# Optimization experiments

Measured on AMD Instinct MI355X. Metric: run time of the kernel, lower is better.

## Reference

```python
import jax, jax.numpy as jnp
import numpy as np
from jax import lax

LBDA = 0.1
EPS = 0.01
NUM_CLASSES = 20


def setup_inputs() -> dict:
    key = jax.random.key(0)
    k1, k2 = jax.random.split(key)
    target_features = jax.random.normal(k1, (2048, 8, 2048), dtype=jnp.float32)
    support_features = jax.random.normal(k2, (100, 8, 2048), dtype=jnp.float32)
    # 20-way 5-shot: every class present so per-class mean is well defined
    support_labels = jnp.repeat(jnp.arange(NUM_CLASSES, dtype=jnp.int32), 100 // NUM_CLASSES)
    return {
        "target_features": target_features,
        "support_features": support_features,
        "support_labels": support_labels,
    }


def _softmin(xs, lbda):
    # -lbda * log(sum_i exp(-x_i/lbda)), stable
    return -lbda * jax.nn.logsumexp(jnp.stack([-x / lbda for x in xs], axis=0), axis=0)


def otam_cum_dist(dists, lbda=LBDA):
    # dists: [Q, Sp, L, S] frame distance matrices
    d = jnp.pad(dists, ((0, 0), (0, 0), (0, 0), (1, 1)))  # pad columns -> M = S + 2
    M = d.shape[-1]
    # row 0: running sum along columns (cum[0,0] = d[0,0] = 0 from padding)
    row0 = jnp.cumsum(d[:, :, 0, :], axis=-1)

    def step(prev_row, d_row):
        # prev_row, d_row: [Q, Sp, M]; column 0 is never written -> stays 0
        cur = [jnp.zeros_like(d_row[..., 0])]
        cur.append(d_row[..., 1] + _softmin([prev_row[..., 0], prev_row[..., 1], cur[0]], lbda))
        for m in range(2, M - 1):
            cur.append(d_row[..., m] + _softmin([prev_row[..., m - 1], cur[m - 1]], lbda))
        cur.append(d_row[..., M - 1] + _softmin([prev_row[..., M - 2], prev_row[..., M - 1], cur[M - 2]], lbda))
        new_row = jnp.stack(cur, axis=-1)
        return new_row, None

    d_rows = jnp.moveaxis(d[:, :, 1:, :], 2, 0)  # [L-1, Q, Sp, M]
    final_row, _ = lax.scan(step, row0, d_rows)
    return final_row[..., -1]  # [Q, Sp]


def cos_sim(x, y, eps=EPS):
    num = x @ y.T
    den = jnp.linalg.norm(x, axis=-1)[:, None] * jnp.linalg.norm(y, axis=-1)[None, :] + eps
    return num / den


def reference(target_features, support_features, support_labels):
    Q, S, D = target_features.shape
    Sp = support_features.shape[0]
    tf = target_features.reshape(Q * S, D)
    sf = support_features.reshape(Sp * S, D)
    frame_dists = 1.0 - cos_sim(tf, sf)  # [Q*S, Sp*S]
    # '(tb ts) (sb ss) -> tb sb ts ss'
    dists = frame_dists.reshape(Q, S, Sp, S).transpose(0, 2, 1, 3)
    cum_dists = otam_cum_dist(dists) + otam_cum_dist(dists.transpose(0, 1, 3, 2))  # [Q, Sp]
    # per-class mean over support (torch.unique returns sorted labels 0..C-1)
    onehot = (support_labels[:, None] == jnp.arange(NUM_CLASSES)[None, :]).astype(cum_dists.dtype)
    onehot = onehot / jnp.sum(onehot, axis=0, keepdims=True)
    class_dists = cum_dists @ onehot  # [Q, C]
    return -class_dists[None]  # logits [1, Q, C]
```

## Files before the change

kernel.cpp:

```cpp
#include <hip/hip_runtime.h>

#define QN    2048
#define SS    8
#define DD    2048
#define SP    100
#define NCLS  20
#define MROWS (QN*SS)
#define NROWS (SP*SS)
#define NPAD  800
#define KK    DD

typedef __bf16 bf16x8 __attribute__((ext_vector_type(8)));
typedef float  f32x4  __attribute__((ext_vector_type(4)));

__device__ __forceinline__ unsigned short f2bf(float f) {
    unsigned int u = __float_as_uint(f);
    u += 0x7fffu + ((u >> 16) & 1u);
    return (unsigned short)(u >> 16);
}

__global__ void cvt_kernel(const float* __restrict__ tf, const float* __restrict__ sf,
                           unsigned short* __restrict__ Abf, unsigned short* __restrict__ Bbf,
                           float* __restrict__ nA, float* __restrict__ nB,
                           float* __restrict__ out)
{
    if (blockIdx.x < 160) out[blockIdx.x * 256 + threadIdx.x] = 0.f;

    const int wv   = threadIdx.x >> 6;
    const int lane = threadIdx.x & 63;
    const int row  = blockIdx.x * 4 + wv;

    const float* src;
    unsigned short* dst;
    float* nrm; int r;
    if (row < MROWS) { src = tf + (size_t)row * DD; dst = Abf + (size_t)row * DD; nrm = nA; r = row; }
    else {
        r = row - MROWS;
        src = sf + (size_t)r * DD; dst = Bbf + (size_t)r * DD; nrm = nB;
    }

    float s = 0.f;
#pragma unroll
    for (int j = 0; j < 8; j++) {
        float4 v = *(const float4*)(src + j * 256 + lane * 4);
        s += v.x*v.x + v.y*v.y + v.z*v.z + v.w*v.w;
        ushort4 pk = make_ushort4(f2bf(v.x), f2bf(v.y), f2bf(v.z), f2bf(v.w));
        *(ushort4*)(dst + j * 256 + lane * 4) = pk;
    }
#pragma unroll
    for (int o = 32; o; o >>= 1) s += __shfl_down(s, o);
    if (lane == 0) nrm[r] = sqrtf(s);
}

__device__ __forceinline__ float softmin2(float a, float b) {
    float mn = fminf(a, b), mx = fmaxf(a, b);
    return mn - 0.1f * __logf(1.0f + __expf((mn - mx) * 10.0f));
}
__device__ __forceinline__ float softmin3(float a, float b, float c) {
    float mn = fminf(fminf(a, b), c);
    float sum = __expf((mn - a) * 10.0f) + __expf((mn - b) * 10.0f) + __expf((mn - c) * 10.0f);
    return mn - 0.1f * __logf(sum);
}

__device__ __forceinline__ void gld16(const void* g, void* l) {
    __builtin_amdgcn_global_load_lds(
        (const __attribute__((address_space(1))) unsigned int*)g,
        (__attribute__((address_space(3))) unsigned int*)l, 16, 0, 0);
}

__device__ __forceinline__ float cellf(const uint4* raw, int a, int b) {
    const unsigned* p = (const unsigned*)raw;
    unsigned wv = p[a * 4 + (b >> 1)];
    return __uint_as_float((b & 1) ? (wv & 0xffff0000u) : (wv << 16));
}

__device__ __forceinline__ float otam_dp(const uint4* raw, int dir) {
    float prev[10], cur[10];
    prev[0] = 0.f;
#pragma unroll
    for (int m = 1; m <= 8; m++) {
        float v0 = cellf(raw, 0, m - 1), v1 = cellf(raw, m - 1, 0);
        prev[m] = prev[m - 1] + (dir ? v1 : v0);
    }
    prev[9] = prev[8];
#pragma unroll
    for (int l = 1; l < 8; l++) {
        float d[8];
#pragma unroll
        for (int j = 0; j < 8; j++) {
            float v0 = cellf(raw, l, j), v1 = cellf(raw, j, l);
            d[j] = dir ? v1 : v0;
        }
        cur[1] = d[0] + softmin3(prev[0], prev[1], 0.0f);
#pragma unroll
        for (int m = 2; m <= 8; m++)
            cur[m] = d[m - 1] + softmin2(prev[m - 1], cur[m - 1]);
        cur[9] = softmin3(prev[8], prev[9], cur[8]);
#pragma unroll
        for (int m = 1; m < 10; m++) prev[m] = cur[m];
    }
    return prev[9];
}

#define EBS (32 * 72)

__global__ __launch_bounds__(256, 2) void gemm_kernel(
    const unsigned short* __restrict__ A,
    const unsigned short* __restrict__ B,
    const float* __restrict__ nA, const float* __restrict__ nB,
    const int* __restrict__ labels,
    float* __restrict__ out)
{
    __shared__ __align__(16) unsigned short smem[4 * EBS];
    unsigned short* Als = smem;
    unsigned short* Bls = smem + 4096;

    const int mt  = blockIdx.x;
    const int nt  = blockIdx.y;
    const int tid = threadIdx.x;
    const int lane = tid & 63;
    const int w    = tid >> 6;
    const int col  = lane & 15, kg = lane >> 4;
    const int mbase0 = mt * 128;

    const int c0 = tid, c1 = tid + 256;
    const unsigned short* Ab0 = A + (size_t)(mbase0 + (c0 >> 2)) * KK + (c0 & 3) * 8;
    const unsigned short* Ab1 = A + (size_t)(mbase0 + (c1 >> 2)) * KK + (c1 & 3) * 8;

    if (nt < 6) {
        const int wm = (w & 1) * 64, wn = (w >> 1) * 64;
        f32x4 acc[4][4] = {};
        const unsigned short* Bb0 = B + (size_t)(nt * 128 + (c0 >> 2)) * KK + (c0 & 3) * 8;
        const unsigned short* Bb1 = B + (size_t)(nt * 128 + (c1 >> 2)) * KK + (c1 & 3) * 8;

        for (int kk = 0; kk < KK; kk += 32) {
            __syncthreads();
            gld16(Ab0 + kk, (char*)Als + c0 * 16);
            gld16(Ab1 + kk, (char*)Als + c1 * 16);
            gld16(Bb0 + kk, (char*)Bls + c0 * 16);
            gld16(Bb1 + kk, (char*)Bls + c1 * 16);
            __syncthreads();
            bf16x8 af[4], bfr[4];
#pragma unroll
            for (int i = 0; i < 4; i++) af[i]  = *(const bf16x8*)(Als + (wm + i * 16 + col) * 32 + kg * 8);
#pragma unroll
            for (int i = 0; i < 4; i++) bfr[i] = *(const bf16x8*)(Bls + (wn + i * 16 + col) * 32 + kg * 8);
#pragma unroll
            for (int mi = 0; mi < 4; mi++)
#pragma unroll
                for (int ni = 0; ni < 4; ni++)
                    acc[mi][ni] = __builtin_amdgcn_mfma_f32_16x16x32_bf16(af[mi], bfr[ni], acc[mi][ni], 0, 0, 0);
        }

        __syncthreads();
        unsigned short* eb = smem + w * EBS;
        const int mbase = mbase0 + wm;
        const int nbase = nt * 128 + wn;
        const int pr  = lane & 31;
        const int qv2 = pr >> 3, sv = pr & 7;
        const int dir = lane >> 5;

#pragma unroll
        for (int p = 0; p < 2; p++) {
            if (p) __syncthreads();
#pragma unroll
            for (int mi2 = 0; mi2 < 2; mi2++) {
                const int mi = p * 2 + mi2;
                float nx[4];
#pragma unroll
                for (int r = 0; r < 4; r++) nx[r] = nA[mbase + mi * 16 + kg * 4 + r];
#pragma unroll
                for (int ni = 0; ni < 4; ni++) {
                    const float ny = nB[nbase + ni * 16 + col];
#pragma unroll
                    for (int r = 0; r < 4; r++) {
                        float d = 1.0f - acc[mi][ni][r] * __builtin_amdgcn_rcpf(nx[r] * ny + 0.01f);
                        eb[(mi2 * 16 + kg * 4 + r) * 72 + ni * 16 + col] = f2bf(d);
                    }
                }
            }
            __syncthreads();

            uint4 raw[8];
            const unsigned short* tb = eb + (qv2 * 8) * 72 + sv * 8;
#pragma unroll
            for (int l = 0; l < 8; l++) raw[l] = *(const uint4*)(tb + l * 72);

            float res = otam_dp(raw, dir);
            res += __shfl_down(res, 32);
            if (dir == 0) {
                const int qg = mt * 16 + (wm >> 3) + p * 4 + qv2;
                const int sg = nt * 16 + (wn >> 3) + sv;
                atomicAdd(out + (size_t)qg * NCLS + labels[sg], -res * 0.2f);
            }
        }
    } else {
        const int wm = w * 32;
        f32x4 acc[2][2] = {};
        const unsigned short* Bb0 = B + (size_t)(768 + (tid >> 2)) * KK + (tid & 3) * 8;

        for (int kk = 0; kk < KK; kk += 32) {
            __syncthreads();
            gld16(Ab0 + kk, (char*)Als + c0 * 16);
            gld16(Ab1 + kk, (char*)Als + c1 * 16);
            if (tid < 128) gld16(Bb0 + kk, (char*)Bls + tid * 16);
            __syncthreads();
            bf16x8 af[2], bfr[2];
#pragma unroll
            for (int i = 0; i < 2; i++) af[i]  = *(const bf16x8*)(Als + (wm + i * 16 + col) * 32 + kg * 8);
#pragma unroll
            for (int i = 0; i < 2; i++) bfr[i] = *(const bf16x8*)(Bls + (i * 16 + col) * 32 + kg * 8);
#pragma unroll
            for (int mi = 0; mi < 2; mi++)
#pragma unroll
                for (int ni = 0; ni < 2; ni++)
                    acc[mi][ni] = __builtin_amdgcn_mfma_f32_16x16x32_bf16(af[mi], bfr[ni], acc[mi][ni], 0, 0, 0);
        }

        __syncthreads();
        unsigned short* eb = smem + w * EBS;
        const int mbase = mbase0 + wm;

#pragma unroll
        for (int mi = 0; mi < 2; mi++) {
            float nx[4];
#pragma unroll
            for (int r = 0; r < 4; r++) nx[r] = nA[mbase + mi * 16 + kg * 4 + r];
#pragma unroll
            for (int ni = 0; ni < 2; ni++) {
                const float ny = nB[768 + ni * 16 + col];
#pragma unroll
                for (int r = 0; r < 4; r++) {
                    float d = 1.0f - acc[mi][ni][r] * __builtin_amdgcn_rcpf(nx[r] * ny + 0.01f);
                    eb[(mi * 16 + kg * 4 + r) * 40 + ni * 16 + col] = f2bf(d);
                }
            }
        }
        __syncthreads();

        const int pr  = lane & 31;
        const int qv2 = (pr & 15) >> 2, sv = pr & 3;
        const int dir = lane >> 5;
        uint4 raw[8];
        const unsigned short* tb = eb + (qv2 * 8) * 40 + sv * 8;
#pragma unroll
        for (int l = 0; l < 8; l++) raw[l] = *(const uint4*)(tb + l * 40);

        float res = otam_dp(raw, dir);
        res += __shfl_down(res, 32);
        if (dir == 0 && pr < 16) {
            const int qg = mt * 16 + w * 4 + qv2;
            const int sg = 96 + sv;
            atomicAdd(out + (size_t)qg * NCLS + labels[sg], -res * 0.2f);
        }
    }
}

extern "C" void kernel_launch(void* const* d_in, const int* in_sizes, int n_in,
                              void* d_out, int out_size, void* d_ws, size_t ws_size,
                              hipStream_t stream)
{
    const float* tf     = (const float*)d_in[0];
    const float* sf     = (const float*)d_in[1];
    const int*   labels = (const int*)d_in[2];
    float* out = (float*)d_out;

    char* ws = (char*)d_ws;
    const size_t szA    = (size_t)MROWS * KK * 2;
    const size_t szB    = (size_t)NPAD  * KK * 2;
    const size_t szNA   = (size_t)MROWS * 4;
    unsigned short* Abf = (unsigned short*)ws;
    unsigned short* Bbf = (unsigned short*)(ws + szA);
    float* nA   = (float*)(ws + szA + szB);
    float* nB   = (float*)(ws + szA + szB + szNA);

    cvt_kernel<<<(MROWS + NPAD) / 4, 256, 0, stream>>>(tf, sf, Abf, Bbf, nA, nB, out);
    gemm_kernel<<<dim3(MROWS / 128, 7), 256, 0, stream>>>(Abf, Bbf, nA, nB, labels, out);
}
```

Baseline: 279.4 us.

## Use 256x256 double-buffered swizzled LDS GEMM tile with padded support rows

Replaces the 128x128 BK=32 GEMM and its separate remainder path with a single 512-thread kernel using 256x256 tiles, BK=64 and double-buffered, XOR-swizzled LDS. Global-to-LDS loads for the next k-step are interleaved with MFMA phases, using fine-grained waitcnt, barriers and setprio. The support matrix is zero-padded to 1024 rows so every tile is full, and out-of-range support columns are masked at the atomic stage. This trades extra padded MMA work and 128KB of dynamic LDS per block for higher data reuse and latency hiding.

New measurement: 281.9 us. Within noise of the previous version (+0.9%).

```diff
diff --git a/kernel.cpp b/kernel.cpp
--- a/kernel.cpp
+++ b/kernel.cpp
@@ -6,9 +6,11 @@
 #define SP    100
 #define NCLS  20
 #define MROWS (QN*SS)
-#define NROWS (SP*SS)
-#define NPAD  800
+#define NREAL (SP*SS)
+#define NPAD  1024
 #define KK    DD
+#define BK    64
+#define NTK   (KK/BK)
 
 typedef __bf16 bf16x8 __attribute__((ext_vector_type(8)));
 typedef float  f32x4  __attribute__((ext_vector_type(4)));
@@ -36,6 +38,14 @@
     if (row < MROWS) { src = tf + (size_t)row * DD; dst = Abf + (size_t)row * DD; nrm = nA; r = row; }
     else {
         r = row - MROWS;
+        if (r >= NREAL) {
+            unsigned short* d2 = Bbf + (size_t)r * DD;
+            ushort4 z = make_ushort4(0, 0, 0, 0);
+#pragma unroll
+            for (int j = 0; j < 8; ++j) *(ushort4*)(d2 + j * 256 + lane * 4) = z;
+            if (lane == 0) nB[r] = 0.f;
+            return;
+        }
         src = sf + (size_t)r * DD; dst = Bbf + (size_t)r * DD; nrm = nB;
     }
 
@@ -102,156 +112,180 @@
     return prev[9];
 }
 
-#define EBS (32 * 72)
-
-__global__ __launch_bounds__(256, 2) void gemm_kernel(
+__global__ __launch_bounds__(512, 2) void gemm_kernel(
     const unsigned short* __restrict__ A,
     const unsigned short* __restrict__ B,
     const float* __restrict__ nA, const float* __restrict__ nB,
     const int* __restrict__ labels,
     float* __restrict__ out)
 {
-    __shared__ __align__(16) unsigned short smem[4 * EBS];
-    unsigned short* Als = smem;
-    unsigned short* Bls = smem + 4096;
-
-    const int mt  = blockIdx.x;
-    const int nt  = blockIdx.y;
-    const int tid = threadIdx.x;
+    extern __shared__ __align__(16) char lds8[];
+
+    const int mt   = blockIdx.x;
+    const int nt   = blockIdx.y;
+    const int tid  = threadIdx.x;
     const int lane = tid & 63;
     const int w    = tid >> 6;
+    const int wm   = w >> 2, wn = w & 3;
     const int col  = lane & 15, kg = lane >> 4;
-    const int mbase0 = mt * 128;
-
-    const int c0 = tid, c1 = tid + 256;
-    const unsigned short* Ab0 = A + (size_t)(mbase0 + (c0 >> 2)) * KK + (c0 & 3) * 8;
-    const unsigned short* Ab1 = A + (size_t)(mbase0 + (c1 >> 2)) * KK + (c1 & 3) * 8;
-
-    if (nt < 6) {
-        const int wm = (w & 1) * 64, wn = (w >> 1) * 64;
-        f32x4 acc[4][4] = {};
-        const unsigned short* Bb0 = B + (size_t)(nt * 128 + (c0 >> 2)) * KK + (c0 & 3) * 8;
-        const unsigned short* Bb1 = B + (size_t)(nt * 128 + (c1 >> 2)) * KK + (c1 & 3) * 8;
-
-        for (int kk = 0; kk < KK; kk += 32) {
-            __syncthreads();
-            gld16(Ab0 + kk, (char*)Als + c0 * 16);
-            gld16(Ab1 + kk, (char*)Als + c1 * 16);
-            gld16(Bb0 + kk, (char*)Bls + c0 * 16);
-            gld16(Bb1 + kk, (char*)Bls + c1 * 16);
-            __syncthreads();
-            bf16x8 af[4], bfr[4];
-#pragma unroll
-            for (int i = 0; i < 4; i++) af[i]  = *(const bf16x8*)(Als + (wm + i * 16 + col) * 32 + kg * 8);
-#pragma unroll
-            for (int i = 0; i < 4; i++) bfr[i] = *(const bf16x8*)(Bls + (wn + i * 16 + col) * 32 + kg * 8);
-#pragma unroll
-            for (int mi = 0; mi < 4; mi++)
-#pragma unroll
-                for (int ni = 0; ni < 4; ni++)
-                    acc[mi][ni] = __builtin_amdgcn_mfma_f32_16x16x32_bf16(af[mi], bfr[ni], acc[mi][ni], 0, 0, 0);
-        }
-
-        __syncthreads();
-        unsigned short* eb = smem + w * EBS;
-        const int mbase = mbase0 + wm;
-        const int nbase = nt * 128 + wn;
-        const int pr  = lane & 31;
-        const int qv2 = pr >> 3, sv = pr & 7;
-        const int dir = lane >> 5;
-
-#pragma unroll
-        for (int p = 0; p < 2; p++) {
-            if (p) __syncthreads();
-#pragma unroll
-            for (int mi2 = 0; mi2 < 2; mi2++) {
-                const int mi = p * 2 + mi2;
-                float nx[4];
-#pragma unroll
-                for (int r = 0; r < 4; r++) nx[r] = nA[mbase + mi * 16 + kg * 4 + r];
-#pragma unroll
-                for (int ni = 0; ni < 4; ni++) {
-                    const float ny = nB[nbase + ni * 16 + col];
-#pragma unroll
-                    for (int r = 0; r < 4; r++) {
-                        float d = 1.0f - acc[mi][ni][r] * __builtin_amdgcn_rcpf(nx[r] * ny + 0.01f);
-                        eb[(mi2 * 16 + kg * 4 + r) * 72 + ni * 16 + col] = f2bf(d);
-                    }
+    const int mbase = mt * 256, nbase = nt * 256;
+
+    const int ks8 = ((lane & 7) ^ (lane >> 3)) << 3;
+    const unsigned short* sA = A + (size_t)(mbase + w * 8 + (lane >> 3)) * KK + ks8;
+    const unsigned short* sB = B + (size_t)(nbase + w * 8 + (lane >> 3)) * KK + ks8;
+    const int stoff = w * 1024 + lane * 16;
+
+    const int sb16 = ((kg ^ (col & 7)) << 4);
+    const int arow = (wm * 128 + col) * 128;
+    const int brow = 32768 + (wn * 64 + col) * 128;
+
+    f32x4 acc[8][4] = {};
+
+    gld16(sB,                       lds8 + 32768 + stoff);
+    gld16(sB + (size_t) 64 * KK,    lds8 + 32768 +  8192 + stoff);
+    gld16(sB + (size_t)128 * KK,    lds8 + 32768 + 16384 + stoff);
+    gld16(sB + (size_t)192 * KK,    lds8 + 32768 + 24576 + stoff);
+    gld16(sA,                       lds8 + stoff);
+    gld16(sA + (size_t)128 * KK,    lds8 + 16384 + stoff);
+    gld16(sA + (size_t) 64 * KK,    lds8 +  8192 + stoff);
+    gld16(sA + (size_t)192 * KK,    lds8 + 24576 + stoff);
+    asm volatile("s_waitcnt vmcnt(0)" ::: "memory");
+    __builtin_amdgcn_s_barrier();
+
+    for (int t = 0; t < NTK; ++t) {
+        const int cb = (t & 1) << 16;
+        const int nb = cb ^ 65536;
+        const bool st = (t + 1 < NTK);
+        const int t1 = (t + 1) * BK;
+        bf16x8 af[4], bf0[4], bf1[4];
+
+#pragma unroll
+        for (int i = 0; i < 4; ++i)
+            af[i]  = *(const bf16x8*)(lds8 + cb + arow + i * 2048 + sb16);
+#pragma unroll
+        for (int n = 0; n < 4; ++n)
+            bf0[n] = *(const bf16x8*)(lds8 + cb + brow + n * 2048 + sb16);
+        if (st) {
+            gld16(sB + t1,                    lds8 + nb + 32768 + stoff);
+            gld16(sB + (size_t) 64 * KK + t1, lds8 + nb + 32768 +  8192 + stoff);
+            gld16(sB + (size_t)128 * KK + t1, lds8 + nb + 32768 + 16384 + stoff);
+            gld16(sB + (size_t)192 * KK + t1, lds8 + nb + 32768 + 24576 + stoff);
+        }
+        __builtin_amdgcn_s_barrier();
+        asm volatile("s_waitcnt lgkmcnt(0)" ::: "memory");
+        __builtin_amdgcn_sched_barrier(0);
+        __builtin_amdgcn_s_setprio(1);
+#pragma unroll
+        for (int mi = 0; mi < 4; ++mi)
+#pragma unroll
+            for (int n = 0; n < 4; ++n)
+                acc[mi][n] = __builtin_amdgcn_mfma_f32_16x16x32_bf16(af[mi], bf0[n], acc[mi][n], 0, 0, 0);
+        __builtin_amdgcn_s_setprio(0);
+        __builtin_amdgcn_sched_barrier(0);
+        __builtin_amdgcn_s_barrier();
+
+#pragma unroll
+        for (int i = 0; i < 4; ++i)
+            af[i]  = *(const bf16x8*)(lds8 + cb + arow + i * 2048 + (sb16 ^ 64));
+#pragma unroll
+        for (int n = 0; n < 4; ++n)
+            bf1[n] = *(const bf16x8*)(lds8 + cb + brow + n * 2048 + (sb16 ^ 64));
+        if (st) {
+            gld16(sA + t1,                    lds8 + nb + stoff);
+            gld16(sA + (size_t)128 * KK + t1, lds8 + nb + 16384 + stoff);
+        }
+        asm volatile("s_waitcnt vmcnt(6)" ::: "memory");
+        __builtin_amdgcn_s_barrier();
+        asm volatile("s_waitcnt lgkmcnt(0)" ::: "memory");
+        __builtin_amdgcn_sched_barrier(0);
+        __builtin_amdgcn_s_setprio(1);
+#pragma unroll
+        for (int mi = 0; mi < 4; ++mi)
+#pragma unroll
+            for (int n = 0; n < 4; ++n)
+                acc[mi][n] = __builtin_amdgcn_mfma_f32_16x16x32_bf16(af[mi], bf1[n], acc[mi][n], 0, 0, 0);
+        __builtin_amdgcn_s_setprio(0);
+        __builtin_amdgcn_sched_barrier(0);
+        __builtin_amdgcn_s_barrier();
+
+#pragma unroll
+        for (int i = 0; i < 4; ++i)
+            af[i] = *(const bf16x8*)(lds8 + cb + arow + 8192 + i * 2048 + sb16);
+        if (st) {
+            gld16(sA + (size_t) 64 * KK + t1, lds8 + nb +  8192 + stoff);
+            gld16(sA + (size_t)192 * KK + t1, lds8 + nb + 24576 + stoff);
+        }
+        __builtin_amdgcn_s_barrier();
+        asm volatile("s_waitcnt lgkmcnt(0)" ::: "memory");
+        __builtin_amdgcn_sched_barrier(0);
+        __builtin_amdgcn_s_setprio(1);
+#pragma unroll
+        for (int mi = 0; mi < 4; ++mi)
+#pragma unroll
+            for (int n = 0; n < 4; ++n)
+                acc[4 + mi][n] = __builtin_amdgcn_mfma_f32_16x16x32_bf16(af[mi], bf0[n], acc[4 + mi][n], 0, 0, 0);
+        __builtin_amdgcn_s_setprio(0);
+        __builtin_amdgcn_sched_barrier(0);
+        __builtin_amdgcn_s_barrier();
+
+#pragma unroll
+        for (int i = 0; i < 4; ++i)
+            af[i] = *(const bf16x8*)(lds8 + cb + arow + 8192 + i * 2048 + (sb16 ^ 64));
+        asm volatile("s_waitcnt vmcnt(2)" ::: "memory");
+        __builtin_amdgcn_s_barrier();
+        asm volatile("s_waitcnt lgkmcnt(0)" ::: "memory");
+        __builtin_amdgcn_sched_barrier(0);
+        __builtin_amdgcn_s_setprio(1);
+#pragma unroll
+        for (int mi = 0; mi < 4; ++mi)
+#pragma unroll
+            for (int n = 0; n < 4; ++n)
+                acc[4 + mi][n] = __builtin_amdgcn_mfma_f32_16x16x32_bf16(af[mi], bf1[n], acc[4 + mi][n], 0, 0, 0);
+        __builtin_amdgcn_s_setprio(0);
+        __builtin_amdgcn_sched_barrier(0);
+        __builtin_amdgcn_s_barrier();
+    }
+
+    __syncthreads();
+    unsigned short* eb = (unsigned short*)lds8 + w * 2304;
+    const int pr  = lane & 31;
+    const int qv2 = pr >> 3, sv = pr & 7;
+    const int dir = lane >> 5;
+
+#pragma unroll
+    for (int p = 0; p < 4; ++p) {
+        if (p) __syncthreads();
+#pragma unroll
+        for (int mi2 = 0; mi2 < 2; ++mi2) {
+            const int mi = p * 2 + mi2;
+            float nx[4];
+#pragma unroll
+            for (int r = 0; r < 4; ++r) nx[r] = nA[mbase + wm * 128 + mi * 16 + kg * 4 + r];
+#pragma unroll
+            for (int ni = 0; ni < 4; ++ni) {
+                const float ny = nB[nbase + wn * 64 + ni * 16 + col];
+#pragma unroll
+                for (int r = 0; r < 4; ++r) {
+                    float d = 1.0f - acc[mi][ni][r] * __builtin_amdgcn_rcpf(nx[r] * ny + 0.01f);
+                    eb[(mi2 * 16 + kg * 4 + r) * 72 + ni * 16 + col] = f2bf(d);
                 }
             }
-            __syncthreads();
-
-            uint4 raw[8];
-            const unsigned short* tb = eb + (qv2 * 8) * 72 + sv * 8;
-#pragma unroll
-            for (int l = 0; l < 8; l++) raw[l] = *(const uint4*)(tb + l * 72);
-
-            float res = otam_dp(raw, dir);
-            res += __shfl_down(res, 32);
-            if (dir == 0) {
-                const int qg = mt * 16 + (wm >> 3) + p * 4 + qv2;
-                const int sg = nt * 16 + (wn >> 3) + sv;
+        }
+        __syncthreads();
+
+        uint4 raw[8];
+        const unsigned short* tb = eb + (qv2 * 8) * 72 + sv * 8;
+#pragma unroll
+        for (int l = 0; l < 8; ++l) raw[l] = *(const uint4*)(tb + l * 72);
+
+        float res = otam_dp(raw, dir);
+        res += __shfl_down(res, 32);
+        if (dir == 0) {
+            const int sg = nt * 32 + wn * 8 + sv;
+            if (sg < SP) {
+                const int qg = mt * 32 + wm * 16 + p * 4 + qv2;
                 atomicAdd(out + (size_t)qg * NCLS + labels[sg], -res * 0.2f);
             }
-        }
-    } else {
-        const int wm = w * 32;
-        f32x4 acc[2][2] = {};
-        const unsigned short* Bb0 = B + (size_t)(768 + (tid >> 2)) * KK + (tid & 3) * 8;
-
-        for (int kk = 0; kk < KK; kk += 32) {
-            __syncthreads();
-            gld16(Ab0 + kk, (char*)Als + c0 * 16);
-            gld16(Ab1 + kk, (char*)Als + c1 * 16);
-            if (tid < 128) gld16(Bb0 + kk, (char*)Bls + tid * 16);
-            __syncthreads();
-            bf16x8 af[2], bfr[2];
-#pragma unroll
-            for (int i = 0; i < 2; i++) af[i]  = *(const bf16x8*)(Als + (wm + i * 16 + col) * 32 + kg * 8);
-#pragma unroll
-            for (int i = 0; i < 2; i++) bfr[i] = *(const bf16x8*)(Bls + (i * 16 + col) * 32 + kg * 8);
-#pragma unroll
-            for (int mi = 0; mi < 2; mi++)
-#pragma unroll
-                for (int ni = 0; ni < 2; ni++)
-                    acc[mi][ni] = __builtin_amdgcn_mfma_f32_16x16x32_bf16(af[mi], bfr[ni], acc[mi][ni], 0, 0, 0);
-        }
-
-        __syncthreads();
-        unsigned short* eb = smem + w * EBS;
-        const int mbase = mbase0 + wm;
-
-#pragma unroll
-        for (int mi = 0; mi < 2; mi++) {
-            float nx[4];
-#pragma unroll
-            for (int r = 0; r < 4; r++) nx[r] = nA[mbase + mi * 16 + kg * 4 + r];
-#pragma unroll
-            for (int ni = 0; ni < 2; ni++) {
-                const float ny = nB[768 + ni * 16 + col];
-#pragma unroll
-                for (int r = 0; r < 4; r++) {
-                    float d = 1.0f - acc[mi][ni][r] * __builtin_amdgcn_rcpf(nx[r] * ny + 0.01f);
-                    eb[(mi * 16 + kg * 4 + r) * 40 + ni * 16 + col] = f2bf(d);
-                }
-            }
-        }
-        __syncthreads();
-
-        const int pr  = lane & 31;
-        const int qv2 = (pr & 15) >> 2, sv = pr & 3;
-        const int dir = lane >> 5;
-        uint4 raw[8];
-        const unsigned short* tb = eb + (qv2 * 8) * 40 + sv * 8;
-#pragma unroll
-        for (int l = 0; l < 8; l++) raw[l] = *(const uint4*)(tb + l * 40);
-
-        float res = otam_dp(raw, dir);
-        res += __shfl_down(res, 32);
-        if (dir == 0 && pr < 16) {
-            const int qg = mt * 16 + w * 4 + qv2;
-            const int sg = 96 + sv;
-            atomicAdd(out + (size_t)qg * NCLS + labels[sg], -res * 0.2f);
         }
     }
 }
@@ -274,6 +308,13 @@
     float* nA   = (float*)(ws + szA + szB);
     float* nB   = (float*)(ws + szA + szB + szNA);
 
+    static int inited = 0;
+    if (!inited) {
+        (void)hipFuncSetAttribute((const void*)gemm_kernel,
+                                  hipFuncAttributeMaxDynamicSharedMemorySize, 131072);
+        inited = 1;
+    }
+
     cvt_kernel<<<(MROWS + NPAD) / 4, 256, 0, stream>>>(tf, sf, Abf, Bbf, nA, nB, out);
-    gemm_kernel<<<dim3(MROWS / 128, 7), 256, 0, stream>>>(Abf, Bbf, nA, nB, labels, out);
-}
+    gemm_kernel<<<dim3(MROWS / 256, NPAD / 256), 512, 131072, stream>>>(Abf, Bbf, nA, nB, labels, out);
+}
```

## Swizzle LDS k-chunks with XOR and remap block order for L2 locality

Applied to the files above, without the earlier changes.

Global-to-LDS loads now place each 16-byte k-chunk at a position XORed with the row index, and the fragment reads use the matching XOR. This is meant to remove LDS bank conflicts when a wavefront reads 16 rows at the same k offset. Block indices are also remapped so that consecutive blocks, spread across the 8 interleaved groups, cover neighbouring M tiles and all N tiles. The aim is better L2/MALL reuse of the A and B tiles. The remap assumes a grid of 128 by 7 blocks.

After: 289.5 us. 3.6% more time.

```diff
diff --git a/kernel.cpp b/kernel.cpp
--- a/kernel.cpp
+++ b/kernel.cpp
@@ -115,23 +115,26 @@
     unsigned short* Als = smem;
     unsigned short* Bls = smem + 4096;
 
-    const int mt  = blockIdx.x;
-    const int nt  = blockIdx.y;
+    const int d   = blockIdx.y * 128 + blockIdx.x;
+    const int s   = (d & 7) * 112 + (d >> 3);
+    const int mt  = s / 7;
+    const int nt  = s % 7;
     const int tid = threadIdx.x;
     const int lane = tid & 63;
     const int w    = tid >> 6;
     const int col  = lane & 15, kg = lane >> 4;
+    const int kgs  = kg ^ (col & 3);
     const int mbase0 = mt * 128;
 
     const int c0 = tid, c1 = tid + 256;
-    const unsigned short* Ab0 = A + (size_t)(mbase0 + (c0 >> 2)) * KK + (c0 & 3) * 8;
-    const unsigned short* Ab1 = A + (size_t)(mbase0 + (c1 >> 2)) * KK + (c1 & 3) * 8;
+    const unsigned short* Ab0 = A + (size_t)(mbase0 + (c0 >> 2)) * KK + (((c0 & 3) ^ ((c0 >> 2) & 3)) * 8);
+    const unsigned short* Ab1 = A + (size_t)(mbase0 + (c1 >> 2)) * KK + (((c1 & 3) ^ ((c1 >> 2) & 3)) * 8);
 
     if (nt < 6) {
         const int wm = (w & 1) * 64, wn = (w >> 1) * 64;
         f32x4 acc[4][4] = {};
-        const unsigned short* Bb0 = B + (size_t)(nt * 128 + (c0 >> 2)) * KK + (c0 & 3) * 8;
-        const unsigned short* Bb1 = B + (size_t)(nt * 128 + (c1 >> 2)) * KK + (c1 & 3) * 8;
+        const unsigned short* Bb0 = B + (size_t)(nt * 128 + (c0 >> 2)) * KK + (((c0 & 3) ^ ((c0 >> 2) & 3)) * 8);
+        const unsigned short* Bb1 = B + (size_t)(nt * 128 + (c1 >> 2)) * KK + (((c1 & 3) ^ ((c1 >> 2) & 3)) * 8);
 
         for (int kk = 0; kk < KK; kk += 32) {
             __syncthreads();
@@ -142,9 +145,9 @@
             __syncthreads();
             bf16x8 af[4], bfr[4];
 #pragma unroll
-            for (int i = 0; i < 4; i++) af[i]  = *(const bf16x8*)(Als + (wm + i * 16 + col) * 32 + kg * 8);
-#pragma unroll
-            for (int i = 0; i < 4; i++) bfr[i] = *(const bf16x8*)(Bls + (wn + i * 16 + col) * 32 + kg * 8);
+            for (int i = 0; i < 4; i++) af[i]  = *(const bf16x8*)(Als + (wm + i * 16 + col) * 32 + kgs * 8);
+#pragma unroll
+            for (int i = 0; i < 4; i++) bfr[i] = *(const bf16x8*)(Bls + (wn + i * 16 + col) * 32 + kgs * 8);
 #pragma unroll
             for (int mi = 0; mi < 4; mi++)
 #pragma unroll
@@ -174,8 +177,8 @@
                     const float ny = nB[nbase + ni * 16 + col];
 #pragma unroll
                     for (int r = 0; r < 4; r++) {
-                        float d = 1.0f - acc[mi][ni][r] * __builtin_amdgcn_rcpf(nx[r] * ny + 0.01f);
-                        eb[(mi2 * 16 + kg * 4 + r) * 72 + ni * 16 + col] = f2bf(d);
+                        float d2 = 1.0f - acc[mi][ni][r] * __builtin_amdgcn_rcpf(nx[r] * ny + 0.01f);
+                        eb[(mi2 * 16 + kg * 4 + r) * 72 + ni * 16 + col] = f2bf(d2);
                     }
                 }
             }
@@ -197,7 +200,7 @@
     } else {
         const int wm = w * 32;
         f32x4 acc[2][2] = {};
-        const unsigned short* Bb0 = B + (size_t)(768 + (tid >> 2)) * KK + (tid & 3) * 8;
+        const unsigned short* Bb0 = B + (size_t)(768 + (tid >> 2)) * KK + (((tid & 3) ^ ((tid >> 2) & 3)) * 8);
 
         for (int kk = 0; kk < KK; kk += 32) {
             __syncthreads();
@@ -207,9 +210,9 @@
             __syncthreads();
             bf16x8 af[2], bfr[2];
 #pragma unroll
-            for (int i = 0; i < 2; i++) af[i]  = *(const bf16x8*)(Als + (wm + i * 16 + col) * 32 + kg * 8);
-#pragma unroll
-            for (int i = 0; i < 2; i++) bfr[i] = *(const bf16x8*)(Bls + (i * 16 + col) * 32 + kg * 8);
+            for (int i = 0; i < 2; i++) af[i]  = *(const bf16x8*)(Als + (wm + i * 16 + col) * 32 + kgs * 8);
+#pragma unroll
+            for (int i = 0; i < 2; i++) bfr[i] = *(const bf16x8*)(Bls + (i * 16 + col) * 32 + kgs * 8);
 #pragma unroll
             for (int mi = 0; mi < 2; mi++)
 #pragma unroll
@@ -231,8 +234,8 @@
                 const float ny = nB[768 + ni * 16 + col];
 #pragma unroll
                 for (int r = 0; r < 4; r++) {
-                    float d = 1.0f - acc[mi][ni][r] * __builtin_amdgcn_rcpf(nx[r] * ny + 0.01f);
-                    eb[(mi * 16 + kg * 4 + r) * 40 + ni * 16 + col] = f2bf(d);
+                    float d2 = 1.0f - acc[mi][ni][r] * __builtin_amdgcn_rcpf(nx[r] * ny + 0.01f);
+                    eb[(mi * 16 + kg * 4 + r) * 40 + ni * 16 + col] = f2bf(d2);
                 }
             }
         }
```
